# Optimization experiments

Measured on AMD Instinct MI355X. Metric: run time of the kernel, lower is better.

## Reference

```python
import jax, jax.numpy as jnp
import numpy as np

N_NODES = 50000


def _gcn_norm(edge_index, num_nodes):
    # PyG gcn_norm with add_self_loops=True, edge_weight=1
    src = jnp.concatenate([edge_index[0], jnp.arange(num_nodes, dtype=edge_index.dtype)])
    dst = jnp.concatenate([edge_index[1], jnp.arange(num_nodes, dtype=edge_index.dtype)])
    deg = jax.ops.segment_sum(jnp.ones_like(dst, dtype=jnp.float32), dst,
                              num_segments=num_nodes)
    deg_inv_sqrt = jnp.where(deg > 0, jax.lax.rsqrt(deg), 0.0)
    norm = deg_inv_sqrt[src] * deg_inv_sqrt[dst]  # [E + N]
    return src, dst, norm


def _gcn_conv(x, src, dst, norm, W, b, num_nodes):
    h = x @ W                                   # [N, F_out] linear first
    msg = h[src] * norm[:, None]                # gather + scale  [E+N, F_out]
    out = jax.ops.segment_sum(msg, dst, num_segments=num_nodes)  # scatter-add
    return out + b


def setup_inputs() -> dict:
    key = jax.random.key(0)
    k1, k2, k3, k4 = jax.random.split(key, 4)
    IN_C, HID, OUT_C, E = 128, 96, 48, 800000
    x = jax.random.normal(k1, (N_NODES, IN_C), dtype=jnp.float32)
    edge_index = jax.random.randint(k2, (2, E), 0, N_NODES, dtype=jnp.int64)
    # Glorot-style scaled weights
    W1 = jax.random.normal(k3, (IN_C, HID), dtype=jnp.float32) * (1.0 / np.sqrt(IN_C))
    b1 = jnp.zeros((HID,), dtype=jnp.float32)
    W2 = jax.random.normal(k4, (HID, OUT_C), dtype=jnp.float32) * (1.0 / np.sqrt(HID))
    b2 = jnp.zeros((OUT_C,), dtype=jnp.float32)
    return {"x": x, "edge_index": edge_index, "W1": W1, "b1": b1, "W2": W2, "b2": b2}


def reference(x, edge_index, W1, b1, W2, b2):
    # cached=True: normalization computed once and reused by both layers
    src, dst, norm = _gcn_norm(edge_index, N_NODES)
    h = jax.nn.relu(_gcn_conv(x, src, dst, norm, W1, b1, N_NODES))
    return _gcn_conv(h, src, dst, norm, W2, b2, N_NODES)
```

## Files before the change

### kernel.cpp

```cpp
#include <hip/hip_runtime.h>

static constexpr int IN_C  = 128;
static constexpr int HID   = 96;
static constexpr int OUT_C = 48;

static constexpr int NPART     = 8;
static constexpr int FILL_ITER = 16;
static constexpr int CHUNK     = 256 * FILL_ITER;

typedef short bf16x8 __attribute__((ext_vector_type(8)));
typedef float f32x4  __attribute__((ext_vector_type(4)));


__device__ __forceinline__ unsigned short f2bf(float f) {
  union { float f; unsigned u; } c; c.f = f;
  unsigned r = c.u + 0x7fffu + ((c.u >> 16) & 1u);
  return (unsigned short)(r >> 16);
}
__device__ __forceinline__ float bflo(unsigned u) {
  union { unsigned u; float f; } c; c.u = u << 16; return c.f;
}
__device__ __forceinline__ float bfhi(unsigned u) {
  union { unsigned u; float f; } c; c.u = u & 0xffff0000u; return c.f;
}

__device__ __forceinline__ void wprep_one(const float* W, uint4* Wt,
                                          int K, int M, int idx) {
  int lane = idx & 63;
  int t = idx >> 6;
  int KB = K / 32;
  int c  = t / KB;
  int kb = t - c * KB;
  int col = c * 16 + (lane & 15);
  int k0  = kb * 32 + (lane >> 4) * 8;
  unsigned pk[4];
#pragma unroll
  for (int q = 0; q < 4; ++q) {
    unsigned lo = f2bf(W[(size_t)(k0 + 2 * q) * M + col]);
    unsigned hi = f2bf(W[(size_t)(k0 + 2 * q + 1) * M + col]);
    pk[q] = lo | (hi << 16);
  }
  Wt[idx] = make_uint4(pk[0], pk[1], pk[2], pk[3]);
}

__global__ void k_init(int* __restrict__ cnt, int n, int nbN,
                       const float* __restrict__ W1, uint4* __restrict__ Wt1, int T1,
                       const float* __restrict__ W2, uint4* __restrict__ Wt2, int T2) {
  int b = blockIdx.x;
  if (b < nbN) {
    int i = b * 256 + threadIdx.x;
    if (i < n) cnt[i] = 0;
  } else {
    int idx = (b - nbN) * 256 + threadIdx.x;
    if (idx < T1) wprep_one(W1, Wt1, IN_C, HID, idx);
    else if (idx < T1 + T2) wprep_one(W2, Wt2, HID, OUT_C, idx - T1);
  }
}


__global__ void k_count(const int* __restrict__ dst, int* __restrict__ cnt,
                        int* __restrict__ perm, int E) {
  int e = blockIdx.x * blockDim.x + threadIdx.x;
  if (e < E) perm[e] = atomicAdd(&cnt[dst[e]], 1);
}

__global__ void k_scan_block(const int* __restrict__ in, int* __restrict__ out_excl,
                             int* __restrict__ bsum, int n) {
  __shared__ int sm[256];
  int i = blockIdx.x * 256 + threadIdx.x;
  int v = (i < n) ? in[i] : 0;
  int val = v;
  sm[threadIdx.x] = val;
  __syncthreads();
  for (int off = 1; off < 256; off <<= 1) {
    int t = (threadIdx.x >= (unsigned)off) ? sm[threadIdx.x - off] : 0;
    __syncthreads();
    val += t;
    sm[threadIdx.x] = val;
    __syncthreads();
  }
  if (i < n) out_excl[i] = val - v;
  if (threadIdx.x == 255) bsum[blockIdx.x] = val;
}

__global__ void k_finish(int* __restrict__ rs, const int* __restrict__ bsum,
                         const int* __restrict__ cnt,
                         float* __restrict__ dinv, int n) {
  __shared__ int sm[256];
  int b = blockIdx.x;
  int t = threadIdx.x;
  int v = (t < b) ? bsum[t] : 0;
  sm[t] = v;
  __syncthreads();
#pragma unroll
  for (int off = 128; off > 0; off >>= 1) {
    if (t < off) sm[t] += sm[t + off];
    __syncthreads();
  }
  int boff = sm[0];
  int i = b * 256 + t;
  if (i < n) {
    rs[i] = rs[i] + boff;
    dinv[i] = rsqrtf((float)cnt[i] + 1.0f);
  }
}


template <int K, int M, bool ABF16>
__device__ __forceinline__ void gemm_body(const void* __restrict__ Xv,
                                          const uint4* __restrict__ Wt,
                                          const float* __restrict__ dinv,
                                          unsigned short* __restrict__ Y,
                                          int N, int gb, unsigned short* lds,
                                          int tid) {
  constexpr int KB = K / 32;
  constexpr int CT = M / 16;
  constexpr int GR = K / 8;
  const int base = gb * 64;

  for (int idx = tid; idx < 64 * GR; idx += 256) {
    int row = idx / GR;
    int g   = idx - row * GR;
    int srow = min(base + row, N - 1);
    uint4 pk;
    if (ABF16) {
      pk = *(const uint4*)((const unsigned short*)Xv + (size_t)srow * K + g * 8);
    } else {
      const float* xp = (const float*)Xv + (size_t)srow * K + g * 8;
      float4 v0 = *(const float4*)xp;
      float4 v1 = *(const float4*)(xp + 4);
      pk.x = (unsigned)f2bf(v0.x) | ((unsigned)f2bf(v0.y) << 16);
      pk.y = (unsigned)f2bf(v0.z) | ((unsigned)f2bf(v0.w) << 16);
      pk.z = (unsigned)f2bf(v1.x) | ((unsigned)f2bf(v1.y) << 16);
      pk.w = (unsigned)f2bf(v1.z) | ((unsigned)f2bf(v1.w) << 16);
    }
    int gs = g ^ (row & 7);
    *(uint4*)(&lds[row * 128 + gs * 8]) = pk;
  }
  __syncthreads();

  const int lane = tid & 63;
  const int wv   = tid >> 6;
  const int lrow = wv * 16 + (lane & 15);
  const int khi  = lane >> 4;

  f32x4 acc[CT];
#pragma unroll
  for (int c = 0; c < CT; ++c) acc[c] = (f32x4){0.f, 0.f, 0.f, 0.f};

  const bf16x8* Wb = (const bf16x8*)Wt;
#pragma unroll
  for (int kb = 0; kb < KB; ++kb) {
    int j  = khi + kb * 4;
    int js = j ^ (lrow & 7);
    bf16x8 a = *(const bf16x8*)(&lds[lrow * 128 + js * 8]);
#pragma unroll
    for (int c = 0; c < CT; ++c) {
      bf16x8 b = Wb[(c * KB + kb) * 64 + lane];
      acc[c] = __builtin_amdgcn_mfma_f32_16x16x32_bf16(a, b, acc[c], 0, 0, 0);
    }
  }

  const int r0 = base + wv * 16 + khi * 4;
#pragma unroll
  for (int i = 0; i < 4; ++i) {
    int row = r0 + i;
    if (row < N) {
      float d = dinv[row];
      unsigned short* yp = Y + (size_t)row * M + (lane & 15);
#pragma unroll
      for (int c = 0; c < CT; ++c) {
        yp[c * 16] = f2bf(acc[c][i] * d);
      }
    }
  }
}

__global__ __launch_bounds__(256) void k_fill_gemm1(
    const int* __restrict__ src, const int* __restrict__ dst,
    const int* __restrict__ perm, const int* __restrict__ rs,
    int* __restrict__ csr, int E, int P, int fillBlocks,
    const float* __restrict__ X, const uint4* __restrict__ Wt,
    const float* __restrict__ dinv, unsigned short* __restrict__ Y, int N) {
  __shared__ unsigned short lds[64 * 128];
  int bid = blockIdx.x;
  if (bid < fillBlocks) {
    int lo = (bid & (NPART - 1)) * P;
    int hi = lo + P;
    int base = (bid >> 3) * CHUNK + threadIdx.x;
#pragma unroll
    for (int i = 0; i < FILL_ITER; ++i) {
      int e = base + i * 256;
      if (e < E) {
        int d = dst[e];
        if (d >= lo && d < hi) {
          csr[rs[d] + perm[e]] = src[e];
        }
      }
    }
    return;
  }
  gemm_body<IN_C, HID, false>(X, Wt, dinv, Y, N, bid - fillBlocks, lds, threadIdx.x);
}

template <int K, int M, bool ABF16>
__global__ __launch_bounds__(256) void k_gemm(const void* __restrict__ Xv,
                                              const uint4* __restrict__ Wt,
                                              const float* __restrict__ dinv,
                                              unsigned short* __restrict__ Y,
                                              int N) {
  __shared__ unsigned short lds[64 * 128];
  gemm_body<K, M, ABF16>(Xv, Wt, dinv, Y, N, blockIdx.x, lds, threadIdx.x);
}


__device__ __forceinline__ void bfacc(float* a, const uint4& v) {
  a[0] += bflo(v.x); a[1] += bfhi(v.x);
  a[2] += bflo(v.y); a[3] += bfhi(v.y);
  a[4] += bflo(v.z); a[5] += bfhi(v.z);
  a[6] += bflo(v.w); a[7] += bfhi(v.w);
}

template <int M, bool RELU, bool OBF16>
__global__ __launch_bounds__(256) void k_agg(const unsigned short* __restrict__ Hs,
                                             const int* __restrict__ csr,
                                             const int* __restrict__ rs,
                                             const int* __restrict__ cnt,
                                             const float* __restrict__ dinv,
                                             const float* __restrict__ bias,
                                             void* __restrict__ outv, int N) {
  constexpr int JC = M / 8;
  int gid = blockIdx.x * blockDim.x + threadIdx.x;
  int n = gid / JC;
  if (n >= N) return;
  int f8 = (gid - n * JC) * 8;
  float dn = dinv[n];
  float a[8] = {};
  {
    uint4 sv = *(const uint4*)(Hs + (size_t)n * M + f8);
    bfacc(a, sv);
  }
  int p = rs[n];
  int e = cnt[n];
  int i = 0;
  for (; i + 8 <= e; i += 8) {
    int s0 = csr[p + i];
    int s1 = csr[p + i + 1];
    int s2 = csr[p + i + 2];
    int s3 = csr[p + i + 3];
    int s4 = csr[p + i + 4];
    int s5 = csr[p + i + 5];
    int s6 = csr[p + i + 6];
    int s7 = csr[p + i + 7];
    uint4 g0 = *(const uint4*)(Hs + (size_t)s0 * M + f8);
    uint4 g1 = *(const uint4*)(Hs + (size_t)s1 * M + f8);
    uint4 g2 = *(const uint4*)(Hs + (size_t)s2 * M + f8);
    uint4 g3 = *(const uint4*)(Hs + (size_t)s3 * M + f8);
    uint4 g4 = *(const uint4*)(Hs + (size_t)s4 * M + f8);
    uint4 g5 = *(const uint4*)(Hs + (size_t)s5 * M + f8);
    uint4 g6 = *(const uint4*)(Hs + (size_t)s6 * M + f8);
    uint4 g7 = *(const uint4*)(Hs + (size_t)s7 * M + f8);
    bfacc(a, g0); bfacc(a, g1); bfacc(a, g2); bfacc(a, g3);
    bfacc(a, g4); bfacc(a, g5); bfacc(a, g6); bfacc(a, g7);
  }
  for (; i + 4 <= e; i += 4) {
    int s0 = csr[p + i];
    int s1 = csr[p + i + 1];
    int s2 = csr[p + i + 2];
    int s3 = csr[p + i + 3];
    uint4 g0 = *(const uint4*)(Hs + (size_t)s0 * M + f8);
    uint4 g1 = *(const uint4*)(Hs + (size_t)s1 * M + f8);
    uint4 g2 = *(const uint4*)(Hs + (size_t)s2 * M + f8);
    uint4 g3 = *(const uint4*)(Hs + (size_t)s3 * M + f8);
    bfacc(a, g0); bfacc(a, g1); bfacc(a, g2); bfacc(a, g3);
  }
  for (; i < e; ++i) {
    int s = csr[p + i];
    uint4 g = *(const uint4*)(Hs + (size_t)s * M + f8);
    bfacc(a, g);
  }
  float r[8];
#pragma unroll
  for (int q = 0; q < 8; ++q) {
    r[q] = fmaf(dn, a[q], bias[f8 + q]);
    if (RELU) r[q] = fmaxf(r[q], 0.0f);
  }
  if (OBF16) {
    uint4 pk;
    pk.x = (unsigned)f2bf(r[0]) | ((unsigned)f2bf(r[1]) << 16);
    pk.y = (unsigned)f2bf(r[2]) | ((unsigned)f2bf(r[3]) << 16);
    pk.z = (unsigned)f2bf(r[4]) | ((unsigned)f2bf(r[5]) << 16);
    pk.w = (unsigned)f2bf(r[6]) | ((unsigned)f2bf(r[7]) << 16);
    *(uint4*)((unsigned short*)outv + (size_t)n * M + f8) = pk;
  } else {
    float* op = (float*)outv + (size_t)n * M + f8;
    *(float4*)(op)     = make_float4(r[0], r[1], r[2], r[3]);
    *(float4*)(op + 4) = make_float4(r[4], r[5], r[6], r[7]);
  }
}


extern "C" void kernel_launch(void* const* d_in, const int* in_sizes, int n_in,
                              void* d_out, int out_size, void* d_ws, size_t ws_size,
                              hipStream_t stream) {
  const float* x  = (const float*)d_in[0];
  const int*   ei = (const int*)d_in[1];
  const float* W1 = (const float*)d_in[2];
  const float* b1 = (const float*)d_in[3];
  const float* W2 = (const float*)d_in[4];
  const float* b2 = (const float*)d_in[5];
  float* out = (float*)d_out;

  const int N = in_sizes[0] / IN_C;
  const int E = in_sizes[1] / 2;
  const int* src = ei;
  const int* dst = ei + E;

  char* ws = (char*)d_ws;
  size_t off = 0;
  auto alloc = [&](size_t bytes) -> void* {
    void* p = ws + off;
    off = (off + bytes + 255) & ~(size_t)255;
    return p;
  };
  int*   cnt    = (int*)alloc((size_t)N * 4);
  int*   rs     = (int*)alloc((size_t)N * 4);
  float* dinv   = (float*)alloc((size_t)N * 4);
  int*   bsum   = (int*)alloc(256 * 4);
  int*   perm   = (int*)alloc((size_t)E * 4);
  int*   csr    = (int*)alloc((size_t)E * 4);
  unsigned short* hbf = (unsigned short*)alloc((size_t)N * HID * 2);
  unsigned short* hb2 = (unsigned short*)alloc((size_t)N * HID * 2);
  constexpr int T1 = (HID / 16) * (IN_C / 32) * 64;
  constexpr int T2 = (OUT_C / 16) * (HID / 32) * 64;
  uint4* Wt1 = (uint4*)alloc((size_t)T1 * 16);
  uint4* Wt2 = (uint4*)alloc((size_t)T2 * 16);

  const int nbN = (N + 255) / 256;
  const int nbE = (E + 255) / 256;
  const int P   = (N + NPART - 1) / NPART;
  const int wprepBlocks = (T1 + T2 + 255) / 256;
  const int fillBlocks  = NPART * ((E + CHUNK - 1) / CHUNK);
  const int rowBlocks   = (N + 63) / 64;

  k_init<<<nbN + wprepBlocks, 256, 0, stream>>>(cnt, N, nbN, W1, Wt1, T1, W2, Wt2, T2);
  k_count<<<nbE, 256, 0, stream>>>(dst, cnt, perm, E);
  k_scan_block<<<nbN, 256, 0, stream>>>(cnt, rs, bsum, N);
  k_finish<<<nbN, 256, 0, stream>>>(rs, bsum, cnt, dinv, N);

  k_fill_gemm1<<<fillBlocks + rowBlocks, 256, 0, stream>>>(
      src, dst, perm, rs, csr, E, P, fillBlocks, x, Wt1, dinv, hbf, N);

  {
    int t = N * (HID / 8);
    k_agg<HID, true, true><<<(t + 255) / 256, 256, 0, stream>>>(hbf, csr, rs, cnt, dinv, b1, hb2, N);
  }
  {
    k_gemm<HID, OUT_C, true><<<rowBlocks, 256, 0, stream>>>(hb2, Wt2, dinv, hbf, N);
    int t = N * (OUT_C / 8);
    k_agg<OUT_C, false, false><<<(t + 255) / 256, 256, 0, stream>>>(hbf, csr, rs, cnt, dinv, b2, out, N);
  }
}
```

Baseline: 128.0 us.

## Fuse layer-1 aggregation with layer-2 GEMM via LDS staging

Layer-1 neighbor aggregation (with bias and ReLU) now writes its bf16 result into shared memory and immediately runs the layer-2 MFMA GEMM in the same block. This removes one kernel launch and the global round trip of the hidden activations. In exchange, each thread now gathers 24 features per neighbor instead of 8, and the edge loop is unrolled only by 2, so there is less parallelism and fewer independent loads in flight for the gather-bound aggregation.

```diff
diff --git a/kernel.cpp b/kernel.cpp
--- a/kernel.cpp
+++ b/kernel.cpp
@@ -107,17 +107,10 @@
 
 
 template <int K, int M, bool ABF16>
-__device__ __forceinline__ void gemm_body(const void* __restrict__ Xv,
-                                          const uint4* __restrict__ Wt,
-                                          const float* __restrict__ dinv,
-                                          unsigned short* __restrict__ Y,
-                                          int N, int gb, unsigned short* lds,
-                                          int tid) {
-  constexpr int KB = K / 32;
-  constexpr int CT = M / 16;
+__device__ __forceinline__ void gemm_stage(const void* __restrict__ Xv,
+                                           int N, int base,
+                                           unsigned short* lds, int tid) {
   constexpr int GR = K / 8;
-  const int base = gb * 64;
-
   for (int idx = tid; idx < 64 * GR; idx += 256) {
     int row = idx / GR;
     int g   = idx - row * GR;
@@ -137,8 +130,16 @@
     int gs = g ^ (row & 7);
     *(uint4*)(&lds[row * 128 + gs * 8]) = pk;
   }
-  __syncthreads();
-
+}
+
+template <int K, int M>
+__device__ __forceinline__ void gemm_compute(const uint4* __restrict__ Wt,
+                                             const float* __restrict__ dinv,
+                                             unsigned short* __restrict__ Y,
+                                             int N, int base,
+                                             const unsigned short* lds, int tid) {
+  constexpr int KB = K / 32;
+  constexpr int CT = M / 16;
   const int lane = tid & 63;
   const int wv   = tid >> 6;
   const int lrow = wv * 16 + (lane & 15);
@@ -175,6 +176,7 @@
     }
   }
 }
+
 
 __global__ __launch_bounds__(256) void k_fill_gemm1(
     const int* __restrict__ src, const int* __restrict__ dst,
@@ -200,17 +202,10 @@
     }
     return;
   }
-  gemm_body<IN_C, HID, false>(X, Wt, dinv, Y, N, bid - fillBlocks, lds, threadIdx.x);
-}
-
-template <int K, int M, bool ABF16>
-__global__ __launch_bounds__(256) void k_gemm(const void* __restrict__ Xv,
-                                              const uint4* __restrict__ Wt,
-                                              const float* __restrict__ dinv,
-                                              unsigned short* __restrict__ Y,
-                                              int N) {
-  __shared__ unsigned short lds[64 * 128];
-  gemm_body<K, M, ABF16>(Xv, Wt, dinv, Y, N, blockIdx.x, lds, threadIdx.x);
+  int gb = bid - fillBlocks;
+  gemm_stage<IN_C, HID, false>(X, N, gb * 64, lds, threadIdx.x);
+  __syncthreads();
+  gemm_compute<IN_C, HID>(Wt, dinv, Y, N, gb * 64, lds, threadIdx.x);
 }
 
 
@@ -221,14 +216,86 @@
   a[6] += bflo(v.w); a[7] += bfhi(v.w);
 }
 
-template <int M, bool RELU, bool OBF16>
-__global__ __launch_bounds__(256) void k_agg(const unsigned short* __restrict__ Hs,
-                                             const int* __restrict__ csr,
-                                             const int* __restrict__ rs,
-                                             const int* __restrict__ cnt,
-                                             const float* __restrict__ dinv,
-                                             const float* __restrict__ bias,
-                                             void* __restrict__ outv, int N) {
+
+__global__ __launch_bounds__(256) void k_agg1_gemm2(
+    const unsigned short* __restrict__ Hs,
+    const int* __restrict__ csr, const int* __restrict__ rs,
+    const int* __restrict__ cnt, const float* __restrict__ dinv,
+    const float* __restrict__ b1, const uint4* __restrict__ Wt2,
+    unsigned short* __restrict__ Y, int N) {
+  __shared__ unsigned short lds[64 * 128];
+  const int tid  = threadIdx.x;
+  const int base = blockIdx.x * 64;
+  const int nl   = tid >> 2;
+  const int fq   = tid & 3;
+  const int n    = base + nl;
+  const int f0   = fq * 24;
+
+  unsigned pk[12];
+  if (n < N) {
+    float dn = dinv[n];
+    float a[24];
+#pragma unroll
+    for (int q = 0; q < 24; ++q) a[q] = 0.f;
+    const unsigned short* hp = Hs + (size_t)n * HID + f0;
+    uint4 s0 = *(const uint4*)(hp);
+    uint4 s1 = *(const uint4*)(hp + 8);
+    uint4 s2 = *(const uint4*)(hp + 16);
+    bfacc(a, s0); bfacc(a + 8, s1); bfacc(a + 16, s2);
+    int p = rs[n];
+    int e = cnt[n];
+    int i = 0;
+    for (; i + 2 <= e; i += 2) {
+      int q0 = csr[p + i];
+      int q1 = csr[p + i + 1];
+      const unsigned short* g0 = Hs + (size_t)q0 * HID + f0;
+      const unsigned short* g1 = Hs + (size_t)q1 * HID + f0;
+      uint4 u0 = *(const uint4*)(g0);
+      uint4 u1 = *(const uint4*)(g0 + 8);
+      uint4 u2 = *(const uint4*)(g0 + 16);
+      uint4 v0 = *(const uint4*)(g1);
+      uint4 v1 = *(const uint4*)(g1 + 8);
+      uint4 v2 = *(const uint4*)(g1 + 16);
+      bfacc(a, u0); bfacc(a + 8, u1); bfacc(a + 16, u2);
+      bfacc(a, v0); bfacc(a + 8, v1); bfacc(a + 16, v2);
+    }
+    for (; i < e; ++i) {
+      int q0 = csr[p + i];
+      const unsigned short* g0 = Hs + (size_t)q0 * HID + f0;
+      uint4 u0 = *(const uint4*)(g0);
+      uint4 u1 = *(const uint4*)(g0 + 8);
+      uint4 u2 = *(const uint4*)(g0 + 16);
+      bfacc(a, u0); bfacc(a + 8, u1); bfacc(a + 16, u2);
+    }
+#pragma unroll
+    for (int q = 0; q < 24; q += 2) {
+      float r0 = fmaxf(fmaf(dn, a[q],     b1[f0 + q]),     0.0f);
+      float r1 = fmaxf(fmaf(dn, a[q + 1], b1[f0 + q + 1]), 0.0f);
+      pk[q / 2] = (unsigned)f2bf(r0) | ((unsigned)f2bf(r1) << 16);
+    }
+  } else {
+#pragma unroll
+    for (int q = 0; q < 12; ++q) pk[q] = 0;
+  }
+#pragma unroll
+  for (int j = 0; j < 3; ++j) {
+    int g  = fq * 3 + j;
+    int gs = g ^ (nl & 7);
+    *(uint4*)(&lds[nl * 128 + gs * 8]) = *(uint4*)(&pk[j * 4]);
+  }
+  __syncthreads();
+  gemm_compute<HID, OUT_C>(Wt2, dinv, Y, N, base, lds, tid);
+}
+
+
+__global__ __launch_bounds__(256) void k_agg2(const unsigned short* __restrict__ Hs,
+                                              const int* __restrict__ csr,
+                                              const int* __restrict__ rs,
+                                              const int* __restrict__ cnt,
+                                              const float* __restrict__ dinv,
+                                              const float* __restrict__ bias,
+                                              float* __restrict__ out, int N) {
+  constexpr int M = OUT_C;
   constexpr int JC = M / 8;
   int gid = blockIdx.x * blockDim.x + threadIdx.x;
   int n = gid / JC;
@@ -279,24 +346,18 @@
     uint4 g = *(const uint4*)(Hs + (size_t)s * M + f8);
     bfacc(a, g);
   }
-  float r[8];
-#pragma unroll
-  for (int q = 0; q < 8; ++q) {
-    r[q] = fmaf(dn, a[q], bias[f8 + q]);
-    if (RELU) r[q] = fmaxf(r[q], 0.0f);
-  }
-  if (OBF16) {
-    uint4 pk;
-    pk.x = (unsigned)f2bf(r[0]) | ((unsigned)f2bf(r[1]) << 16);
-    pk.y = (unsigned)f2bf(r[2]) | ((unsigned)f2bf(r[3]) << 16);
-    pk.z = (unsigned)f2bf(r[4]) | ((unsigned)f2bf(r[5]) << 16);
-    pk.w = (unsigned)f2bf(r[6]) | ((unsigned)f2bf(r[7]) << 16);
-    *(uint4*)((unsigned short*)outv + (size_t)n * M + f8) = pk;
-  } else {
-    float* op = (float*)outv + (size_t)n * M + f8;
-    *(float4*)(op)     = make_float4(r[0], r[1], r[2], r[3]);
-    *(float4*)(op + 4) = make_float4(r[4], r[5], r[6], r[7]);
-  }
+  float4 r0, r1;
+  r0.x = fmaf(dn, a[0], bias[f8 + 0]);
+  r0.y = fmaf(dn, a[1], bias[f8 + 1]);
+  r0.z = fmaf(dn, a[2], bias[f8 + 2]);
+  r0.w = fmaf(dn, a[3], bias[f8 + 3]);
+  r1.x = fmaf(dn, a[4], bias[f8 + 4]);
+  r1.y = fmaf(dn, a[5], bias[f8 + 5]);
+  r1.z = fmaf(dn, a[6], bias[f8 + 6]);
+  r1.w = fmaf(dn, a[7], bias[f8 + 7]);
+  float* op = out + (size_t)n * M + f8;
+  *(float4*)(op)     = r0;
+  *(float4*)(op + 4) = r1;
 }
 
 
@@ -351,13 +412,10 @@
   k_fill_gemm1<<<fillBlocks + rowBlocks, 256, 0, stream>>>(
       src, dst, perm, rs, csr, E, P, fillBlocks, x, Wt1, dinv, hbf, N);
 
+  k_agg1_gemm2<<<rowBlocks, 256, 0, stream>>>(hbf, csr, rs, cnt, dinv, b1, Wt2, hb2, N);
+
   {
-    int t = N * (HID / 8);
-    k_agg<HID, true, true><<<(t + 255) / 256, 256, 0, stream>>>(hbf, csr, rs, cnt, dinv, b1, hb2, N);
-  }
-  {
-    k_gemm<HID, OUT_C, true><<<rowBlocks, 256, 0, stream>>>(hb2, Wt2, dinv, hbf, N);
     int t = N * (OUT_C / 8);
-    k_agg<OUT_C, false, false><<<(t + 255) / 256, 256, 0, stream>>>(hbf, csr, rs, cnt, dinv, b2, out, N);
-  }
-}
+    k_agg2<<<(t + 255) / 256, 256, 0, stream>>>(hb2, csr, rs, cnt, dinv, b2, out, N);
+  }
+}
```

Result: faster. 124.4 us (-2.8%).
